# Kernel tuning notes

Measured on AMD Instinct MI355X. Metric: run time of the kernel, lower is better.

## Reference

```python
import jax, jax.numpy as jnp
import numpy as np


def _gcn_conv(x, edge_index, W, b):
    # PyG GCNConv: add self loops, symmetric normalization D^-1/2 (A+I) D^-1/2, then linear.
    N = x.shape[0]
    src, dst = edge_index[0], edge_index[1]
    deg = jax.ops.segment_sum(jnp.ones(src.shape[0], x.dtype), dst, num_segments=N) + 1.0
    dinv = jax.lax.rsqrt(deg)  # [N]
    xw = x @ W  # [N, H]
    msg = xw[src] * (dinv[src] * dinv[dst])[:, None]  # [E, H] gathered messages
    agg = jax.ops.segment_sum(msg, dst, num_segments=N)
    agg = agg + xw * (dinv * dinv)[:, None]  # self-loop contribution
    return agg + b


def setup_inputs() -> dict:
    key = jax.random.key(0)
    ks = jax.random.split(key, 10)
    N, E, R = 100_000, 1_600_000, 10_000
    Cin, H, Cout = 64, 64, 1
    x = jax.random.normal(ks[0], (N, Cin), jnp.float32)
    edge_index = jax.random.randint(ks[1], (2, E), 0, N, dtype=jnp.int32)
    edge_attr = jax.random.normal(ks[2], (E, 2), jnp.float32)
    # contiguous route ranges covering [0, E)
    cuts = jnp.sort(jax.random.randint(ks[3], (R - 1,), 0, E, dtype=jnp.int32))
    starts = jnp.concatenate([jnp.zeros((1,), cuts.dtype), cuts])
    ends = jnp.concatenate([cuts, jnp.full((1,), E, cuts.dtype)])
    route_indices = jnp.stack([starts, ends], axis=1)  # [R, 2]
    W1 = jax.random.normal(ks[4], (Cin, H), jnp.float32) / np.sqrt(Cin)
    b1 = jnp.zeros((H,), jnp.float32)
    W2 = jax.random.normal(ks[5], (H, H), jnp.float32) / np.sqrt(H)
    b2 = jnp.zeros((H,), jnp.float32)
    Wfc = jax.random.normal(ks[6], (H + 2, Cout), jnp.float32) / np.sqrt(H + 2)
    bfc = jnp.zeros((Cout,), jnp.float32)
    return dict(x=x, edge_attr=edge_attr, W1=W1, b1=b1, W2=W2, b2=b2,
                Wfc=Wfc, bfc=bfc, edge_index=edge_index, route_indices=route_indices)


def reference(x, edge_attr, W1, b1, W2, b2, Wfc, bfc, edge_index, route_indices):
    h = jax.nn.relu(_gcn_conv(x, edge_index, W1, b1))
    h = jax.nn.relu(_gcn_conv(h, edge_index, W2, b2))
    src = edge_index[0]
    H = h.shape[1]
    # fc(concat([h[src], edge_attr])) without materializing the concat
    pred = h[src] @ Wfc[:H] + edge_attr @ Wfc[H:] + bfc  # [E, Cout]
    pred = pred.sum(axis=1)  # route_pred sums over all fc outputs
    E = src.shape[0]
    starts, ends = route_indices[:, 0], route_indices[:, 1]
    eidx = jnp.arange(E)
    # map each edge to its route segment (ranges are sorted & contiguous)
    seg = jnp.clip(jnp.searchsorted(starts, eidx, side='right') - 1, 0, starts.shape[0] - 1)
    valid = (eidx >= starts[seg]) & (eidx < ends[seg])
    return jax.ops.segment_sum(jnp.where(valid, pred, 0.0), seg,
                               num_segments=route_indices.shape[0])
```

## Files before the change

kernel.cpp:

```cpp
#include <hip/hip_runtime.h>
#include <hip/hip_bf16.h>

typedef unsigned int uint32;
typedef unsigned short ushort;
typedef __attribute__((ext_vector_type(8))) short bf16x8;
typedef __attribute__((ext_vector_type(4))) float f32x4;

#define CAP 64
#define BSZ 512
#define REGION 16384

__device__ __forceinline__ ushort f2bf(float f) {
    unsigned int u = __float_as_uint(f);
    unsigned int r = (u + 0x7FFFu + ((u >> 16) & 1u)) >> 16;
    return (ushort)r;
}
__device__ __forceinline__ float bf_lo(uint32 v) {
    return __uint_as_float(v << 16);
}
__device__ __forceinline__ float bf_hi(uint32 v) {
    return __uint_as_float(v & 0xFFFF0000u);
}
__device__ __forceinline__ bf16x8 pack8(float4 p, float4 q) {
    bf16x8 r;
    r[0] = (short)f2bf(p.x); r[1] = (short)f2bf(p.y);
    r[2] = (short)f2bf(p.z); r[3] = (short)f2bf(p.w);
    r[4] = (short)f2bf(q.x); r[5] = (short)f2bf(q.y);
    r[6] = (short)f2bf(q.z); r[7] = (short)f2bf(q.w);
    return r;
}

__global__ __launch_bounds__(256) void prep_w(const float* __restrict__ W1,
                                              const float* __restrict__ W2,
                                              ushort* __restrict__ wb1,
                                              ushort* __restrict__ wb2,
                                              int* __restrict__ cur, int nbkt) {
    int idx = blockIdx.x * 256 + threadIdx.x;
    if (idx < nbkt) cur[idx] = idx * REGION;
    int e = idx & 7;
    int lane = (idx >> 3) & 63;
    int kk = (idx >> 9) & 1;
    int colT = (idx >> 10) & 3;
    int k = kk * 32 + (lane >> 4) * 8 + e;
    int cc = colT * 16 + (lane & 15);
    wb1[idx] = f2bf(W1[k * 64 + cc]);
    wb2[idx] = f2bf(W2[k * 64 + cc]);
}

__global__ __launch_bounds__(256) void scatter_k(const int* __restrict__ src,
                                                 const int* __restrict__ dst,
                                                 int* __restrict__ cur,
                                                 uint32* __restrict__ buf,
                                                 int E, int nbkt) {
    __shared__ int lcnt[256];
    __shared__ int lbase[256];
    int t = threadIdx.x;
    if (t < 256) lcnt[t] = 0;
    __syncthreads();

    int base = (blockIdx.x * 256 + t) * 8;
    int s[8], d[8], r[8];
    if (base + 8 <= E) {
        int4 sv0 = *(const int4*)(&src[base]);
        int4 sv1 = *(const int4*)(&src[base + 4]);
        int4 dv0 = *(const int4*)(&dst[base]);
        int4 dv1 = *(const int4*)(&dst[base + 4]);
        s[0] = sv0.x; s[1] = sv0.y; s[2] = sv0.z; s[3] = sv0.w;
        s[4] = sv1.x; s[5] = sv1.y; s[6] = sv1.z; s[7] = sv1.w;
        d[0] = dv0.x; d[1] = dv0.y; d[2] = dv0.z; d[3] = dv0.w;
        d[4] = dv1.x; d[5] = dv1.y; d[6] = dv1.z; d[7] = dv1.w;
    } else {
#pragma unroll
        for (int j = 0; j < 8; ++j) {
            int e = base + j;
            s[j] = (e < E) ? src[e] : 0;
            d[j] = (e < E) ? dst[e] : -1;
        }
    }
#pragma unroll
    for (int j = 0; j < 8; ++j) {
        if (d[j] >= 0) r[j] = atomicAdd(&lcnt[d[j] >> 9], 1);
    }
    __syncthreads();
    if (t < nbkt && lcnt[t] > 0) lbase[t] = atomicAdd(&cur[t], lcnt[t]);
    __syncthreads();
#pragma unroll
    for (int j = 0; j < 8; ++j) {
        if (d[j] >= 0) {
            int bkt = d[j] >> 9;
            int idx = lbase[bkt] + r[j];
            if (idx < (bkt + 1) * REGION)
                buf[idx] = ((uint32)s[j] << 9) | (uint32)(d[j] & (BSZ - 1));
        }
    }
}

__global__ __launch_bounds__(256) void fill_bucket(const uint32* __restrict__ buf,
                                                   const int* __restrict__ cur,
                                                   int* __restrict__ col,
                                                   int* __restrict__ cnt,
                                                   float* __restrict__ dinv,
                                                   int N) {
    __shared__ int lcnt[BSZ];
    int b = blockIdx.x;
    int t = threadIdx.x;
    for (int i = t; i < BSZ; i += 256) lcnt[i] = 0;
    __syncthreads();

    int base = b * REGION;
    int end = cur[b];
    int cap = base + REGION;
    if (end > cap) end = cap;
    int node0 = b << 9;
    for (int i = base + t; i < end; i += 256) {
        uint32 u = buf[i];
        int d = (int)(u & (BSZ - 1));
        int s = (int)(u >> 9);
        int slot = atomicAdd(&lcnt[d], 1);
        if (slot < CAP) col[(size_t)(node0 + d) * CAP + slot] = s;
    }
    __syncthreads();
    for (int d = t; d < BSZ; d += 256) {
        int gd = node0 + d;
        if (gd < N) {
            int c = lcnt[d];
            cnt[gd] = c;
            dinv[gd] = rsqrtf((float)c + 1.0f);
        }
    }
}

__global__ __launch_bounds__(256) void gemm_mfma_x(const float* __restrict__ x,
                                                   const ushort* __restrict__ wb,
                                                   const float* __restrict__ dinv,
                                                   ushort* __restrict__ out, int N) {
    int t = threadIdx.x;
    int w = t >> 6, l = t & 63;
    int row0 = blockIdx.x * 64 + w * 16;
    int lr = l & 15, tq = l >> 4;
    int ar = row0 + lr;
    int arc = ar < N ? ar : N - 1;

    const float* xr = x + (size_t)arc * 64 + tq * 8;
    float4 p0 = *(const float4*)(xr);
    float4 p1 = *(const float4*)(xr + 4);
    float4 q0 = *(const float4*)(xr + 32);
    float4 q1 = *(const float4*)(xr + 36);
    bf16x8 a0 = pack8(p0, p1);
    bf16x8 a1 = pack8(q0, q1);

    const uint4* wb4 = (const uint4*)wb;
    f32x4 acc[4];
#pragma unroll
    for (int c = 0; c < 4; ++c) {
        f32x4 z = {0.f, 0.f, 0.f, 0.f};
        bf16x8 b0 = __builtin_bit_cast(bf16x8, wb4[(c * 2 + 0) * 64 + l]);
        bf16x8 b1 = __builtin_bit_cast(bf16x8, wb4[(c * 2 + 1) * 64 + l]);
        z = __builtin_amdgcn_mfma_f32_16x16x32_bf16(a0, b0, z, 0, 0, 0);
        z = __builtin_amdgcn_mfma_f32_16x16x32_bf16(a1, b1, z, 0, 0, 0);
        acc[c] = z;
    }
#pragma unroll
    for (int r = 0; r < 4; ++r) {
        int g = row0 + tq * 4 + r;
        if (g < N) {
            float dv = dinv[g];
#pragma unroll
            for (int c = 0; c < 4; ++c)
                out[(size_t)g * 64 + c * 16 + lr] = f2bf(acc[c][r] * dv);
        }
    }
}

__device__ __forceinline__ void agg_gather8(const uint32* __restrict__ yt,
                                            const int* __restrict__ colrow,
                                            int wid, int nb,
                                            int lane, float acc[8]) {
    int s = lane >> 3;
    int c = lane & 7;
    int cvl = (lane < nb) ? colrow[lane] : -1;
#pragma unroll
    for (int j = 0; j < 8; ++j) acc[j] = 0.f;
    int m = nb + 1;
    int nbat = (m + 7) >> 3;

    auto one = [&](int b) {
        int j = 8 * b + s;
        int sl = j - 1;
        int rr = __shfl(cvl, sl < 0 ? 0 : sl);
        int r = (j == 0) ? wid : ((j >= m) ? -1 : rr);
        if (r >= 0) {
            uint4 v = *(const uint4*)(yt + (size_t)r * 32 + 4 * c);
            acc[0] += bf_lo(v.x); acc[1] += bf_hi(v.x);
            acc[2] += bf_lo(v.y); acc[3] += bf_hi(v.y);
            acc[4] += bf_lo(v.z); acc[5] += bf_hi(v.z);
            acc[6] += bf_lo(v.w); acc[7] += bf_hi(v.w);
        }
    };
    int b = 0;
    for (; b + 3 <= nbat; b += 3) { one(b); one(b + 1); one(b + 2); }
    for (; b < nbat; ++b) one(b);

#pragma unroll
    for (int j = 0; j < 8; ++j) {
        acc[j] += __shfl_xor(acc[j], 8);
        acc[j] += __shfl_xor(acc[j], 16);
        acc[j] += __shfl_xor(acc[j], 32);
    }
}

__global__ __launch_bounds__(256) void agg_z2_kernel(const uint32* __restrict__ y1,
                                                     const int* __restrict__ cnt,
                                                     const int* __restrict__ col,
                                                     const float* __restrict__ dinv,
                                                     const float* __restrict__ bias,
                                                     const ushort* __restrict__ wb,
                                                     ushort* __restrict__ y2, int N) {
    int t = threadIdx.x;
    int wid = blockIdx.x * 4 + (t >> 6);
    int lane = t & 63;
    if (wid >= N) return;
    int nb = cnt[wid];
    nb = nb > CAP ? CAP : nb;
    float acc[8];
    agg_gather8(y1, col + (size_t)wid * CAP, wid, nb, lane, acc);

    float di = dinv[wid];
    int c = lane & 7;
    float4 bv0 = *(const float4*)(&bias[8 * c]);
    float4 bv1 = *(const float4*)(&bias[8 * c + 4]);
    float h[8];
    h[0] = acc[0] * di + bv0.x; h[1] = acc[1] * di + bv0.y;
    h[2] = acc[2] * di + bv0.z; h[3] = acc[3] * di + bv0.w;
    h[4] = acc[4] * di + bv1.x; h[5] = acc[5] * di + bv1.y;
    h[6] = acc[6] * di + bv1.z; h[7] = acc[7] * di + bv1.w;
    uint32 pk[4];
#pragma unroll
    for (int j = 0; j < 4; ++j) {
        float a = h[2 * j] > 0.f ? h[2 * j] : 0.f;
        float b = h[2 * j + 1] > 0.f ? h[2 * j + 1] : 0.f;
        pk[j] = (uint32)f2bf(a * di) | ((uint32)f2bf(b * di) << 16);
    }
    int tq = lane >> 4;
    uint32 a0u[4], a1u[4];
#pragma unroll
    for (int j = 0; j < 4; ++j) {
        a0u[j] = __shfl(pk[j], tq);
        a1u[j] = __shfl(pk[j], 4 + tq);
    }
    bool valid = (lane & 15) == 0;
#pragma unroll
    for (int j = 0; j < 4; ++j) {
        a0u[j] = valid ? a0u[j] : 0u;
        a1u[j] = valid ? a1u[j] : 0u;
    }
    bf16x8 a0 = __builtin_bit_cast(bf16x8, make_uint4(a0u[0], a0u[1], a0u[2], a0u[3]));
    bf16x8 a1 = __builtin_bit_cast(bf16x8, make_uint4(a1u[0], a1u[1], a1u[2], a1u[3]));

    const uint4* wb4 = (const uint4*)wb;
    float out4[4];
#pragma unroll
    for (int c4 = 0; c4 < 4; ++c4) {
        f32x4 zz = {0.f, 0.f, 0.f, 0.f};
        bf16x8 b0 = __builtin_bit_cast(bf16x8, wb4[(c4 * 2 + 0) * 64 + lane]);
        bf16x8 b1 = __builtin_bit_cast(bf16x8, wb4[(c4 * 2 + 1) * 64 + lane]);
        zz = __builtin_amdgcn_mfma_f32_16x16x32_bf16(a0, b0, zz, 0, 0, 0);
        zz = __builtin_amdgcn_mfma_f32_16x16x32_bf16(a1, b1, zz, 0, 0, 0);
        out4[c4] = zz[0];
    }
    if (tq == 0) {
#pragma unroll
        for (int c4 = 0; c4 < 4; ++c4)
            y2[(size_t)wid * 64 + c4 * 16 + lane] = f2bf(out4[c4]);
    }
}

__global__ __launch_bounds__(256) void agg_nv_kernel(const uint32* __restrict__ y2,
                                                     const int* __restrict__ cnt,
                                                     const int* __restrict__ col,
                                                     const float* __restrict__ dinv,
                                                     const float* __restrict__ bias,
                                                     const float* __restrict__ wfc,
                                                     float* __restrict__ nv, int N) {
    int t = threadIdx.x;
    int wid = blockIdx.x * 4 + (t >> 6);
    int lane = t & 63;
    if (wid >= N) return;
    int c = lane & 7;
    int nb = cnt[wid];
    nb = nb > CAP ? CAP : nb;
    float acc[8];
    agg_gather8(y2, col + (size_t)wid * CAP, wid, nb, lane, acc);

    float di = dinv[wid];
    float4 bv0 = *(const float4*)(&bias[8 * c]);
    float4 bv1 = *(const float4*)(&bias[8 * c + 4]);
    float4 wv0 = *(const float4*)(&wfc[8 * c]);
    float4 wv1 = *(const float4*)(&wfc[8 * c + 4]);
    float p = 0.f, h;
    h = acc[0] * di + bv0.x; p += (h > 0.f ? h : 0.f) * wv0.x;
    h = acc[1] * di + bv0.y; p += (h > 0.f ? h : 0.f) * wv0.y;
    h = acc[2] * di + bv0.z; p += (h > 0.f ? h : 0.f) * wv0.z;
    h = acc[3] * di + bv0.w; p += (h > 0.f ? h : 0.f) * wv0.w;
    h = acc[4] * di + bv1.x; p += (h > 0.f ? h : 0.f) * wv1.x;
    h = acc[5] * di + bv1.y; p += (h > 0.f ? h : 0.f) * wv1.y;
    h = acc[6] * di + bv1.z; p += (h > 0.f ? h : 0.f) * wv1.z;
    h = acc[7] * di + bv1.w; p += (h > 0.f ? h : 0.f) * wv1.w;
    p += __shfl_xor(p, 1);
    p += __shfl_xor(p, 2);
    p += __shfl_xor(p, 4);
    if (lane == 0) nv[wid] = p;
}

__global__ __launch_bounds__(256) void route_kernel(const float* __restrict__ nv,
                                                    const int* __restrict__ src,
                                                    const float* __restrict__ ea,
                                                    const float* __restrict__ wfc,
                                                    const float* __restrict__ bfc,
                                                    const int* __restrict__ routes,
                                                    float* __restrict__ out, int R) {
    int r = blockIdx.x * 4 + (threadIdx.x >> 6);
    int lane = threadIdx.x & 63;
    if (r >= R) return;
    int s0 = routes[2 * r], s1 = routes[2 * r + 1];
    float w0 = wfc[64], w1 = wfc[65], b = bfc[0];
    float acc = 0.f;
    for (int e = s0 + lane; e < s1; e += 64) {
        float2 a = *(const float2*)(&ea[2 * (size_t)e]);
        acc += nv[src[e]] + a.x * w0 + a.y * w1 + b;
    }
#pragma unroll
    for (int off = 32; off; off >>= 1) acc += __shfl_down(acc, off);
    if (lane == 0) out[r] = acc;
}

extern "C" void kernel_launch(void* const* d_in, const int* in_sizes, int n_in,
                              void* d_out, int out_size, void* d_ws, size_t ws_size,
                              hipStream_t stream) {
    const float* x   = (const float*)d_in[0];
    const float* ea  = (const float*)d_in[1];
    const float* W1  = (const float*)d_in[2];
    const float* b1  = (const float*)d_in[3];
    const float* W2  = (const float*)d_in[4];
    const float* b2  = (const float*)d_in[5];
    const float* Wfc = (const float*)d_in[6];
    const float* bfc = (const float*)d_in[7];
    const int* eidx  = (const int*)d_in[8];
    const int* routes= (const int*)d_in[9];

    int N = in_sizes[0] / 64;
    int E = in_sizes[8] / 2;
    int R = in_sizes[9] / 2;
    const int* src = eidx;
    const int* dst = eidx + E;
    int nbkt = (N + BSZ - 1) / BSZ;

    char* ws = (char*)d_ws;
    size_t off = 0;
    auto alloc = [&](size_t bytes) -> void* {
        off = (off + 255) & ~(size_t)255;
        void* p = ws + off;
        off += bytes;
        return p;
    };

    float*  dinv = (float*)alloc((size_t)N * 4);
    int*    cnt  = (int*)alloc((size_t)N * 4);
    int*    cur  = (int*)alloc((size_t)nbkt * 4);
    uint32* buf  = (uint32*)alloc((size_t)nbkt * REGION * 4);
    int*    col  = (int*)alloc((size_t)N * CAP * 4);
    ushort* y1   = (ushort*)alloc((size_t)N * 64 * 2);
    ushort* y2   = (ushort*)alloc((size_t)N * 64 * 2);
    float*  nv   = (float*)alloc((size_t)N * 4);
    ushort* wb1  = (ushort*)alloc(4096 * 2);
    ushort* wb2  = (ushort*)alloc(4096 * 2);

    int eb8 = (E + 2047) / 2048;

    prep_w<<<16, 256, 0, stream>>>(W1, W2, wb1, wb2, cur, nbkt);

    scatter_k<<<eb8, 256, 0, stream>>>(src, dst, cur, buf, E, nbkt);
    fill_bucket<<<nbkt, 256, 0, stream>>>(buf, cur, col, cnt, dinv, N);

    gemm_mfma_x<<<(N + 63) / 64, 256, 0, stream>>>(x, wb1, dinv, y1, N);
    agg_z2_kernel<<<(N + 3) / 4, 256, 0, stream>>>((const uint32*)y1, cnt, col, dinv, b1, wb2, y2, N);
    agg_nv_kernel<<<(N + 3) / 4, 256, 0, stream>>>((const uint32*)y2, cnt, col, dinv, b2, Wfc, nv, N);

    route_kernel<<<(R + 3) / 4, 256, 0, stream>>>(nv, src, ea, Wfc, bfc, routes, (float*)d_out, R);
}
```

Baseline: 178.2 us.

## Process two nodes per wavefront in aggregation kernels; scatter 16 edges per thread

The two aggregation kernels now assign a pair of destination nodes to each wavefront. The neighbour gathers for both nodes are interleaved so more loads are in flight per wave, and the layer-2 MFMA fills two A rows instead of one, halving the number of matrix ops per node. The edge scatter kernel also handles 16 edges per thread instead of 8, which halves its block count and the global atomics on bucket cursors. The cost is higher register pressure, possible loss of occupancy, and lanes idling when the two nodes' degrees differ.

```diff
diff --git a/kernel.cpp b/kernel.cpp
--- a/kernel.cpp
+++ b/kernel.cpp
@@ -58,34 +58,33 @@
     if (t < 256) lcnt[t] = 0;
     __syncthreads();
 
-    int base = (blockIdx.x * 256 + t) * 8;
-    int s[8], d[8], r[8];
-    if (base + 8 <= E) {
-        int4 sv0 = *(const int4*)(&src[base]);
-        int4 sv1 = *(const int4*)(&src[base + 4]);
-        int4 dv0 = *(const int4*)(&dst[base]);
-        int4 dv1 = *(const int4*)(&dst[base + 4]);
-        s[0] = sv0.x; s[1] = sv0.y; s[2] = sv0.z; s[3] = sv0.w;
-        s[4] = sv1.x; s[5] = sv1.y; s[6] = sv1.z; s[7] = sv1.w;
-        d[0] = dv0.x; d[1] = dv0.y; d[2] = dv0.z; d[3] = dv0.w;
-        d[4] = dv1.x; d[5] = dv1.y; d[6] = dv1.z; d[7] = dv1.w;
+    int base = (blockIdx.x * 256 + t) * 16;
+    int s[16], d[16], r[16];
+    if (base + 16 <= E) {
+#pragma unroll
+        for (int q = 0; q < 4; ++q) {
+            int4 sv = *(const int4*)(&src[base + 4 * q]);
+            int4 dv = *(const int4*)(&dst[base + 4 * q]);
+            s[4 * q] = sv.x; s[4 * q + 1] = sv.y; s[4 * q + 2] = sv.z; s[4 * q + 3] = sv.w;
+            d[4 * q] = dv.x; d[4 * q + 1] = dv.y; d[4 * q + 2] = dv.z; d[4 * q + 3] = dv.w;
+        }
     } else {
 #pragma unroll
-        for (int j = 0; j < 8; ++j) {
+        for (int j = 0; j < 16; ++j) {
             int e = base + j;
             s[j] = (e < E) ? src[e] : 0;
             d[j] = (e < E) ? dst[e] : -1;
         }
     }
 #pragma unroll
-    for (int j = 0; j < 8; ++j) {
+    for (int j = 0; j < 16; ++j) {
         if (d[j] >= 0) r[j] = atomicAdd(&lcnt[d[j] >> 9], 1);
     }
     __syncthreads();
     if (t < nbkt && lcnt[t] > 0) lbase[t] = atomicAdd(&cur[t], lcnt[t]);
     __syncthreads();
 #pragma unroll
-    for (int j = 0; j < 8; ++j) {
+    for (int j = 0; j < 16; ++j) {
         if (d[j] >= 0) {
             int bkt = d[j] >> 9;
             int idx = lbase[bkt] + r[j];
@@ -172,40 +171,64 @@
     }
 }
 
-__device__ __forceinline__ void agg_gather8(const uint32* __restrict__ yt,
-                                            const int* __restrict__ colrow,
-                                            int wid, int nb,
-                                            int lane, float acc[8]) {
+__device__ __forceinline__ void agg_gather8_dual(const uint32* __restrict__ yt,
+                                                 const int* __restrict__ col,
+                                                 int wid0, int nbA,
+                                                 int wid1, int nbB,
+                                                 int lane,
+                                                 float accA[8], float accB[8]) {
     int s = lane >> 3;
     int c = lane & 7;
-    int cvl = (lane < nb) ? colrow[lane] : -1;
-#pragma unroll
-    for (int j = 0; j < 8; ++j) acc[j] = 0.f;
-    int m = nb + 1;
-    int nbat = (m + 7) >> 3;
-
-    auto one = [&](int b) {
+    const int* rowA = col + (size_t)wid0 * CAP;
+    const int* rowB = col + (size_t)wid1 * CAP;
+    int cvlA = (lane < nbA) ? rowA[lane] : -1;
+    int cvlB = (nbB > 0 && lane < nbB) ? rowB[lane] : -1;
+#pragma unroll
+    for (int j = 0; j < 8; ++j) { accA[j] = 0.f; accB[j] = 0.f; }
+    int mA = nbA + 1;
+    int mB = (nbB >= 0) ? nbB + 1 : 0;
+    int nbatA = (mA + 7) >> 3;
+    int nbatB = (mB + 7) >> 3;
+    int nbat = nbatA > nbatB ? nbatA : nbatB;
+
+    auto oneA = [&](int b) {
         int j = 8 * b + s;
         int sl = j - 1;
-        int rr = __shfl(cvl, sl < 0 ? 0 : sl);
-        int r = (j == 0) ? wid : ((j >= m) ? -1 : rr);
+        int rr = __shfl(cvlA, sl < 0 ? 0 : sl);
+        int r = (j == 0) ? wid0 : ((j >= mA) ? -1 : rr);
         if (r >= 0) {
             uint4 v = *(const uint4*)(yt + (size_t)r * 32 + 4 * c);
-            acc[0] += bf_lo(v.x); acc[1] += bf_hi(v.x);
-            acc[2] += bf_lo(v.y); acc[3] += bf_hi(v.y);
-            acc[4] += bf_lo(v.z); acc[5] += bf_hi(v.z);
-            acc[6] += bf_lo(v.w); acc[7] += bf_hi(v.w);
+            accA[0] += bf_lo(v.x); accA[1] += bf_hi(v.x);
+            accA[2] += bf_lo(v.y); accA[3] += bf_hi(v.y);
+            accA[4] += bf_lo(v.z); accA[5] += bf_hi(v.z);
+            accA[6] += bf_lo(v.w); accA[7] += bf_hi(v.w);
         }
     };
-    int b = 0;
-    for (; b + 3 <= nbat; b += 3) { one(b); one(b + 1); one(b + 2); }
-    for (; b < nbat; ++b) one(b);
-
+    auto oneB = [&](int b) {
+        int j = 8 * b + s;
+        int sl = j - 1;
+        int rr = __shfl(cvlB, sl < 0 ? 0 : sl);
+        int r = (j == 0) ? wid1 : ((j >= mB) ? -1 : rr);
+        if (r >= 0) {
+            uint4 v = *(const uint4*)(yt + (size_t)r * 32 + 4 * c);
+            accB[0] += bf_lo(v.x); accB[1] += bf_hi(v.x);
+            accB[2] += bf_lo(v.y); accB[3] += bf_hi(v.y);
+            accB[4] += bf_lo(v.z); accB[5] += bf_hi(v.z);
+            accB[6] += bf_lo(v.w); accB[7] += bf_hi(v.w);
+        }
+    };
+    for (int b = 0; b < nbat; ++b) {
+        if (b < nbatA) oneA(b);
+        if (b < nbatB) oneB(b);
+    }
 #pragma unroll
     for (int j = 0; j < 8; ++j) {
-        acc[j] += __shfl_xor(acc[j], 8);
-        acc[j] += __shfl_xor(acc[j], 16);
-        acc[j] += __shfl_xor(acc[j], 32);
+        accA[j] += __shfl_xor(accA[j], 8);
+        accA[j] += __shfl_xor(accA[j], 16);
+        accA[j] += __shfl_xor(accA[j], 32);
+        accB[j] += __shfl_xor(accB[j], 8);
+        accB[j] += __shfl_xor(accB[j], 16);
+        accB[j] += __shfl_xor(accB[j], 32);
     }
 }
 
@@ -217,48 +240,59 @@
                                                      const ushort* __restrict__ wb,
                                                      ushort* __restrict__ y2, int N) {
     int t = threadIdx.x;
-    int wid = blockIdx.x * 4 + (t >> 6);
+    int pair = blockIdx.x * 4 + (t >> 6);
+    int wid0 = pair * 2, wid1 = wid0 + 1;
     int lane = t & 63;
-    if (wid >= N) return;
-    int nb = cnt[wid];
-    nb = nb > CAP ? CAP : nb;
-    float acc[8];
-    agg_gather8(y1, col + (size_t)wid * CAP, wid, nb, lane, acc);
-
-    float di = dinv[wid];
+    if (wid0 >= N) return;
+    bool hasB = wid1 < N;
+    int nbA = cnt[wid0]; nbA = nbA > CAP ? CAP : nbA;
+    int nbB = hasB ? cnt[wid1] : -1; nbB = nbB > CAP ? CAP : nbB;
+    float accA[8], accB[8];
+    agg_gather8_dual(y1, col, wid0, nbA, wid1, nbB, lane, accA, accB);
+
+    float diA = dinv[wid0];
+    float diB = hasB ? dinv[wid1] : 0.f;
     int c = lane & 7;
     float4 bv0 = *(const float4*)(&bias[8 * c]);
     float4 bv1 = *(const float4*)(&bias[8 * c + 4]);
-    float h[8];
-    h[0] = acc[0] * di + bv0.x; h[1] = acc[1] * di + bv0.y;
-    h[2] = acc[2] * di + bv0.z; h[3] = acc[3] * di + bv0.w;
-    h[4] = acc[4] * di + bv1.x; h[5] = acc[5] * di + bv1.y;
-    h[6] = acc[6] * di + bv1.z; h[7] = acc[7] * di + bv1.w;
-    uint32 pk[4];
+    uint32 pkA[4], pkB[4];
+    {
+        float h[8];
+        h[0] = accA[0] * diA + bv0.x; h[1] = accA[1] * diA + bv0.y;
+        h[2] = accA[2] * diA + bv0.z; h[3] = accA[3] * diA + bv0.w;
+        h[4] = accA[4] * diA + bv1.x; h[5] = accA[5] * diA + bv1.y;
+        h[6] = accA[6] * diA + bv1.z; h[7] = accA[7] * diA + bv1.w;
+#pragma unroll
+        for (int j = 0; j < 4; ++j) {
+            float a = h[2 * j] > 0.f ? h[2 * j] : 0.f;
+            float b = h[2 * j + 1] > 0.f ? h[2 * j + 1] : 0.f;
+            pkA[j] = (uint32)f2bf(a * diA) | ((uint32)f2bf(b * diA) << 16);
+        }
+        h[0] = accB[0] * diB + bv0.x; h[1] = accB[1] * diB + bv0.y;
+        h[2] = accB[2] * diB + bv0.z; h[3] = accB[3] * diB + bv0.w;
+        h[4] = accB[4] * diB + bv1.x; h[5] = accB[5] * diB + bv1.y;
+        h[6] = accB[6] * diB + bv1.z; h[7] = accB[7] * diB + bv1.w;
+#pragma unroll
+        for (int j = 0; j < 4; ++j) {
+            float a = h[2 * j] > 0.f ? h[2 * j] : 0.f;
+            float b = h[2 * j + 1] > 0.f ? h[2 * j + 1] : 0.f;
+            pkB[j] = (uint32)f2bf(a * diB) | ((uint32)f2bf(b * diB) << 16);
+        }
+    }
+    int row = lane & 15, tq = lane >> 4;
+    uint32 a0u[4], a1u[4];
 #pragma unroll
     for (int j = 0; j < 4; ++j) {
-        float a = h[2 * j] > 0.f ? h[2 * j] : 0.f;
-        float b = h[2 * j + 1] > 0.f ? h[2 * j + 1] : 0.f;
-        pk[j] = (uint32)f2bf(a * di) | ((uint32)f2bf(b * di) << 16);
-    }
-    int tq = lane >> 4;
-    uint32 a0u[4], a1u[4];
-#pragma unroll
-    for (int j = 0; j < 4; ++j) {
-        a0u[j] = __shfl(pk[j], tq);
-        a1u[j] = __shfl(pk[j], 4 + tq);
-    }
-    bool valid = (lane & 15) == 0;
-#pragma unroll
-    for (int j = 0; j < 4; ++j) {
-        a0u[j] = valid ? a0u[j] : 0u;
-        a1u[j] = valid ? a1u[j] : 0u;
+        uint32 A0 = __shfl(pkA[j], tq),     B0 = __shfl(pkB[j], tq);
+        uint32 A1 = __shfl(pkA[j], 4 + tq), B1 = __shfl(pkB[j], 4 + tq);
+        a0u[j] = (row == 0) ? A0 : ((row == 1) ? B0 : 0u);
+        a1u[j] = (row == 0) ? A1 : ((row == 1) ? B1 : 0u);
     }
     bf16x8 a0 = __builtin_bit_cast(bf16x8, make_uint4(a0u[0], a0u[1], a0u[2], a0u[3]));
     bf16x8 a1 = __builtin_bit_cast(bf16x8, make_uint4(a1u[0], a1u[1], a1u[2], a1u[3]));
 
     const uint4* wb4 = (const uint4*)wb;
-    float out4[4];
+    float out0[4], out1[4];
 #pragma unroll
     for (int c4 = 0; c4 < 4; ++c4) {
         f32x4 zz = {0.f, 0.f, 0.f, 0.f};
@@ -266,12 +300,18 @@
         bf16x8 b1 = __builtin_bit_cast(bf16x8, wb4[(c4 * 2 + 1) * 64 + lane]);
         zz = __builtin_amdgcn_mfma_f32_16x16x32_bf16(a0, b0, zz, 0, 0, 0);
         zz = __builtin_amdgcn_mfma_f32_16x16x32_bf16(a1, b1, zz, 0, 0, 0);
-        out4[c4] = zz[0];
+        out0[c4] = zz[0];
+        out1[c4] = zz[1];
     }
     if (tq == 0) {
 #pragma unroll
         for (int c4 = 0; c4 < 4; ++c4)
-            y2[(size_t)wid * 64 + c4 * 16 + lane] = f2bf(out4[c4]);
+            y2[(size_t)wid0 * 64 + c4 * 16 + lane] = f2bf(out0[c4]);
+        if (hasB) {
+#pragma unroll
+            for (int c4 = 0; c4 < 4; ++c4)
+                y2[(size_t)wid1 * 64 + c4 * 16 + lane] = f2bf(out1[c4]);
+        }
     }
 }
 
@@ -283,33 +323,47 @@
                                                      const float* __restrict__ wfc,
                                                      float* __restrict__ nv, int N) {
     int t = threadIdx.x;
-    int wid = blockIdx.x * 4 + (t >> 6);
+    int pair = blockIdx.x * 4 + (t >> 6);
+    int wid0 = pair * 2, wid1 = wid0 + 1;
     int lane = t & 63;
-    if (wid >= N) return;
+    if (wid0 >= N) return;
+    bool hasB = wid1 < N;
+    int nbA = cnt[wid0]; nbA = nbA > CAP ? CAP : nbA;
+    int nbB = hasB ? cnt[wid1] : -1; nbB = nbB > CAP ? CAP : nbB;
+    float accA[8], accB[8];
+    agg_gather8_dual(y2, col, wid0, nbA, wid1, nbB, lane, accA, accB);
+
+    float diA = dinv[wid0];
+    float diB = hasB ? dinv[wid1] : 0.f;
     int c = lane & 7;
-    int nb = cnt[wid];
-    nb = nb > CAP ? CAP : nb;
-    float acc[8];
-    agg_gather8(y2, col + (size_t)wid * CAP, wid, nb, lane, acc);
-
-    float di = dinv[wid];
     float4 bv0 = *(const float4*)(&bias[8 * c]);
     float4 bv1 = *(const float4*)(&bias[8 * c + 4]);
     float4 wv0 = *(const float4*)(&wfc[8 * c]);
     float4 wv1 = *(const float4*)(&wfc[8 * c + 4]);
-    float p = 0.f, h;
-    h = acc[0] * di + bv0.x; p += (h > 0.f ? h : 0.f) * wv0.x;
-    h = acc[1] * di + bv0.y; p += (h > 0.f ? h : 0.f) * wv0.y;
-    h = acc[2] * di + bv0.z; p += (h > 0.f ? h : 0.f) * wv0.z;
-    h = acc[3] * di + bv0.w; p += (h > 0.f ? h : 0.f) * wv0.w;
-    h = acc[4] * di + bv1.x; p += (h > 0.f ? h : 0.f) * wv1.x;
-    h = acc[5] * di + bv1.y; p += (h > 0.f ? h : 0.f) * wv1.y;
-    h = acc[6] * di + bv1.z; p += (h > 0.f ? h : 0.f) * wv1.z;
-    h = acc[7] * di + bv1.w; p += (h > 0.f ? h : 0.f) * wv1.w;
-    p += __shfl_xor(p, 1);
-    p += __shfl_xor(p, 2);
-    p += __shfl_xor(p, 4);
-    if (lane == 0) nv[wid] = p;
+    float pA = 0.f, pB = 0.f, h;
+    h = accA[0] * diA + bv0.x; pA += (h > 0.f ? h : 0.f) * wv0.x;
+    h = accA[1] * diA + bv0.y; pA += (h > 0.f ? h : 0.f) * wv0.y;
+    h = accA[2] * diA + bv0.z; pA += (h > 0.f ? h : 0.f) * wv0.z;
+    h = accA[3] * diA + bv0.w; pA += (h > 0.f ? h : 0.f) * wv0.w;
+    h = accA[4] * diA + bv1.x; pA += (h > 0.f ? h : 0.f) * wv1.x;
+    h = accA[5] * diA + bv1.y; pA += (h > 0.f ? h : 0.f) * wv1.y;
+    h = accA[6] * diA + bv1.z; pA += (h > 0.f ? h : 0.f) * wv1.z;
+    h = accA[7] * diA + bv1.w; pA += (h > 0.f ? h : 0.f) * wv1.w;
+    h = accB[0] * diB + bv0.x; pB += (h > 0.f ? h : 0.f) * wv0.x;
+    h = accB[1] * diB + bv0.y; pB += (h > 0.f ? h : 0.f) * wv0.y;
+    h = accB[2] * diB + bv0.z; pB += (h > 0.f ? h : 0.f) * wv0.z;
+    h = accB[3] * diB + bv0.w; pB += (h > 0.f ? h : 0.f) * wv0.w;
+    h = accB[4] * diB + bv1.x; pB += (h > 0.f ? h : 0.f) * wv1.x;
+    h = accB[5] * diB + bv1.y; pB += (h > 0.f ? h : 0.f) * wv1.y;
+    h = accB[6] * diB + bv1.z; pB += (h > 0.f ? h : 0.f) * wv1.z;
+    h = accB[7] * diB + bv1.w; pB += (h > 0.f ? h : 0.f) * wv1.w;
+    pA += __shfl_xor(pA, 1); pB += __shfl_xor(pB, 1);
+    pA += __shfl_xor(pA, 2); pB += __shfl_xor(pB, 2);
+    pA += __shfl_xor(pA, 4); pB += __shfl_xor(pB, 4);
+    if (lane == 0) {
+        nv[wid0] = pA;
+        if (hasB) nv[wid1] = pB;
+    }
 }
 
 __global__ __launch_bounds__(256) void route_kernel(const float* __restrict__ nv,
@@ -375,16 +429,16 @@
     ushort* wb1  = (ushort*)alloc(4096 * 2);
     ushort* wb2  = (ushort*)alloc(4096 * 2);
 
-    int eb8 = (E + 2047) / 2048;
+    int eb16 = (E + 4095) / 4096;
 
     prep_w<<<16, 256, 0, stream>>>(W1, W2, wb1, wb2, cur, nbkt);
 
-    scatter_k<<<eb8, 256, 0, stream>>>(src, dst, cur, buf, E, nbkt);
+    scatter_k<<<eb16, 256, 0, stream>>>(src, dst, cur, buf, E, nbkt);
     fill_bucket<<<nbkt, 256, 0, stream>>>(buf, cur, col, cnt, dinv, N);
 
     gemm_mfma_x<<<(N + 63) / 64, 256, 0, stream>>>(x, wb1, dinv, y1, N);
-    agg_z2_kernel<<<(N + 3) / 4, 256, 0, stream>>>((const uint32*)y1, cnt, col, dinv, b1, wb2, y2, N);
-    agg_nv_kernel<<<(N + 3) / 4, 256, 0, stream>>>((const uint32*)y2, cnt, col, dinv, b2, Wfc, nv, N);
+    agg_z2_kernel<<<(N + 7) / 8, 256, 0, stream>>>((const uint32*)y1, cnt, col, dinv, b1, wb2, y2, N);
+    agg_nv_kernel<<<(N + 7) / 8, 256, 0, stream>>>((const uint32*)y2, cnt, col, dinv, b2, Wfc, nv, N);
 
     route_kernel<<<(R + 3) / 4, 256, 0, stream>>>(nv, src, ea, Wfc, bfc, routes, (float*)d_out, R);
 }
```

New measurement: 164.0 us, median of 2. 1.09x faster.
